# Optimization experiments

Hardware: AMD Instinct MI355X
Metric: run time of the kernel (lower is better)

## Reference

```python
import jax, jax.numpy as jnp
import numpy as np

MAX_FRAMES = 12
EMBED_DIM = 512
TOPK = 12
NUM_SAMPLES = 500
SIGMA = 0.05
SEL_DIM = 2
NUM_HEADS = 2


def setup_inputs() -> dict:
    key = jax.random.key(0)
    ks = jax.random.split(key, 9)
    D = EMBED_DIM
    C = D // 2
    s = lambda fan_in: 1.0 / np.sqrt(fan_in)
    return {
        "x": jax.random.normal(ks[0], (16, MAX_FRAMES * 50, D), dtype=jnp.float32),
        "ln_g": jnp.ones((D,), jnp.float32),
        "ln_b": jnp.zeros((D,), jnp.float32),
        "w_in": jax.random.normal(ks[1], (D, C), jnp.float32) * s(D),
        "wq": jax.random.normal(ks[2], (C, C), jnp.float32) * s(C),
        "wk": jax.random.normal(ks[3], (C, C), jnp.float32) * s(C),
        "wv": jax.random.normal(ks[4], (C, C), jnp.float32) * s(C),
        "wo": jax.random.normal(ks[5], (C, C), jnp.float32) * s(C),
        "w1": jax.random.normal(ks[6], (2 * C, C), jnp.float32) * s(2 * C),
        "w2": jax.random.normal(ks[7], (C, 1), jnp.float32) * s(C),
    }


def layer_norm(x, g, b, eps=1e-5):
    mu = jnp.mean(x, axis=-1, keepdims=True)
    var = jnp.var(x, axis=-1, keepdims=True)
    return (x - mu) * jax.lax.rsqrt(var + eps) * g + b


def mha(x, wq, wk, wv, wo):
    B, N, C = x.shape
    hd = C // NUM_HEADS
    q = (x @ wq).reshape(B, N, NUM_HEADS, hd).transpose(0, 2, 1, 3)
    k = (x @ wk).reshape(B, N, NUM_HEADS, hd).transpose(0, 2, 1, 3)
    v = (x @ wv).reshape(B, N, NUM_HEADS, hd).transpose(0, 2, 1, 3)
    attn = jax.nn.softmax(jnp.einsum('bhnd,bhmd->bhnm', q, k) / np.sqrt(hd), axis=-1)
    out = jnp.einsum('bhnm,bhmd->bhnd', attn, v).transpose(0, 2, 1, 3).reshape(B, N, C)
    return out @ wo


def predictor(x, ln_g, ln_b, w_in, wq, wk, wv, wo, w1, w2):
    h = jax.nn.gelu(layer_norm(x, ln_g, ln_b) @ w_in, approximate=False)
    h = mha(h, wq, wk, wv, wo)
    B, N, C = h.shape
    g = jnp.mean(h, axis=1, keepdims=True)
    h = jnp.concatenate([h, jnp.broadcast_to(g, (B, N, C))], axis=-1)
    h = jax.nn.gelu(h @ w1, approximate=False)
    return jnp.tanh(h @ w2)  # (B, N, 1)


def perturbed_topk(scores):
    # scores: (b, d) -> soft indicators (b, k, d)
    b, d = scores.shape
    noise = jax.random.normal(jax.random.key(1), (b, NUM_SAMPLES, d), dtype=scores.dtype)
    perturbed = scores[:, None, :] + noise * SIGMA
    _, idx = jax.lax.top_k(perturbed, TOPK)            # (b, ns, k)
    idx = jnp.sort(idx, axis=-1)
    onehot = jax.nn.one_hot(idx, d, dtype=scores.dtype)  # (b, ns, k, d)
    return onehot.mean(axis=1)                          # (b, k, d)


def reference(x, ln_g, ln_b, w_in, wq, wk, wv, wo, w1, w2):
    B, L, D = x.shape
    N = L // MAX_FRAMES
    xf = x.reshape(B * MAX_FRAMES, N, D)
    pred = predictor(xf, ln_g, ln_b, w_in, wq, wk, wv, wo, w1, w2)[..., 0]  # (b, N)
    spatial_score = pred[:, SEL_DIM:]                    # (b, N-2)
    ind = perturbed_topk(spatial_score)                  # (b, k, N-2)
    cls_feat = xf[:, :SEL_DIM, :]
    spatial_feat = xf[:, SEL_DIM:, :]
    sel = jnp.einsum('bkl,bld->bkd', ind, spatial_feat)
    out = jnp.concatenate([cls_feat, sel], axis=1)       # (b, 2+k, D)
    return out.reshape(B, -1, D)
```

## Files before the change

### kernel.cpp

```cpp
#include <hip/hip_runtime.h>
#include <stdint.h>

#define B2      192
#define NTOK    50
#define ROWS    9600
#define D_EMB   512
#define C_DIM   256
#define HD      128
#define NSAMP   500
#define TOPKK   12
#define NSPA    48

typedef short short8 __attribute__((ext_vector_type(8)));
typedef float f32x4  __attribute__((ext_vector_type(4)));

__device__ __forceinline__ float gelu_f(float x) {
    return 0.5f * x * (1.0f + erff(x * 0.7071067811865476f));
}
__device__ __forceinline__ uint16_t f2bf(float x) {
    uint32_t u = __float_as_uint(x);
    return (uint16_t)((u + 0x7fffu + ((u >> 16) & 1u)) >> 16);
}
__device__ __forceinline__ float bf2f(uint16_t b) {
    return __uint_as_float(((uint32_t)b) << 16);
}
__device__ __forceinline__ size_t swzA(int m, int k, int K) {
    return ((size_t)(m >> 4) * (K >> 5) + (k >> 5)) * 512
         + (size_t)((((k >> 3) & 3) * 16 + (m & 15)) * 8 + (k & 7));
}

__global__ __launch_bounds__(256) void prep_kernel(const float* __restrict__ x,
                                                   const float* __restrict__ g,
                                                   const float* __restrict__ b,
                                                   short* __restrict__ xh,
                                                   short* __restrict__ xl,
                                                   const float* __restrict__ w_in, const float* __restrict__ wq,
                                                   const float* __restrict__ wk, const float* __restrict__ wv,
                                                   const float* __restrict__ wo, const float* __restrict__ w1,
                                                   short* win_hi, short* win_lo, short* wq_hi, short* wq_lo,
                                                   short* wk_hi, short* wk_lo, short* wv_hi, short* wv_lo,
                                                   short* wo_hi, short* wo_lo, short* w1a_hi, short* w1a_lo,
                                                   short* w1b_hi, short* w1b_lo) {
    if (blockIdx.x < 2400) {
        int row  = blockIdx.x * 4 + (threadIdx.x >> 6);
        int lane = threadIdx.x & 63;
        const float* rp = x + (size_t)row * D_EMB;
        float4 v0 = *(const float4*)(rp + lane * 8);
        float4 v1 = *(const float4*)(rp + lane * 8 + 4);
        float s  = v0.x + v0.y + v0.z + v0.w + v1.x + v1.y + v1.z + v1.w;
        float s2 = v0.x*v0.x + v0.y*v0.y + v0.z*v0.z + v0.w*v0.w
                 + v1.x*v1.x + v1.y*v1.y + v1.z*v1.z + v1.w*v1.w;
#pragma unroll
        for (int off = 32; off; off >>= 1) {
            s  += __shfl_xor(s,  off);
            s2 += __shfl_xor(s2, off);
        }
        float mu  = s / 512.0f;
        float var = s2 / 512.0f - mu * mu;
        float inv = 1.0f / sqrtf(var + 1e-5f);
        const float* gp = g + lane * 8;
        const float* bp = b + lane * 8;
        float o[8];
        o[0]=(v0.x-mu)*inv*gp[0]+bp[0]; o[1]=(v0.y-mu)*inv*gp[1]+bp[1];
        o[2]=(v0.z-mu)*inv*gp[2]+bp[2]; o[3]=(v0.w-mu)*inv*gp[3]+bp[3];
        o[4]=(v1.x-mu)*inv*gp[4]+bp[4]; o[5]=(v1.y-mu)*inv*gp[5]+bp[5];
        o[6]=(v1.z-mu)*inv*gp[6]+bp[6]; o[7]=(v1.w-mu)*inv*gp[7]+bp[7];
        short8 h8, l8;
#pragma unroll
        for (int j = 0; j < 8; ++j) {
            uint16_t h = f2bf(o[j]);
            h8[j] = (short)h;
            l8[j] = (short)f2bf(o[j] - bf2f(h));
        }
        size_t blk = (size_t)(row >> 4) * 16 + (lane >> 2);
        int inner  = (lane & 3) * 16 + (row & 15);
        ((short8*)xh)[blk * 64 + inner] = h8;
        ((short8*)xl)[blk * 64 + inner] = l8;
    } else {
        int blk = blockIdx.x - 2400;
        const float* W; short *hi, *lo; int K, base;
        if      (blk <  64) { W = w_in;            hi = win_hi; lo = win_lo; K = 512; base = 0;   }
        else if (blk <  96) { W = wq;              hi = wq_hi;  lo = wq_lo;  K = 256; base = 64;  }
        else if (blk < 128) { W = wk;              hi = wk_hi;  lo = wk_lo;  K = 256; base = 96;  }
        else if (blk < 160) { W = wv;              hi = wv_hi;  lo = wv_lo;  K = 256; base = 128; }
        else if (blk < 192) { W = wo;              hi = wo_hi;  lo = wo_lo;  K = 256; base = 160; }
        else if (blk < 224) { W = w1;              hi = w1a_hi; lo = w1a_lo; K = 256; base = 192; }
        else                { W = w1 + 256 * 256;  hi = w1b_hi; lo = w1b_lo; K = 256; base = 224; }
        int t = (blk - base) * 256 + threadIdx.x;
        int n = t & 255, k8 = t >> 8;
        short8 h8, l8;
#pragma unroll
        for (int j = 0; j < 8; ++j) {
            float wvl = W[(size_t)(k8 * 8 + j) * 256 + n];
            uint16_t h = f2bf(wvl);
            h8[j] = (short)h;
            l8[j] = (short)f2bf(wvl - bf2f(h));
        }
        size_t bb = (size_t)(n >> 4) * (K >> 5) + (k8 >> 2);
        int inner = (k8 & 3) * 16 + (n & 15);
        ((short8*)hi)[bb * 64 + inner] = h8;
        ((short8*)lo)[bb * 64 + inner] = l8;
    }
}

template<int KB>
__device__ __forceinline__ void mm_core(const short8* __restrict__ pAh, const short8* __restrict__ pAl,
                                        const short8* __restrict__ pBh0, const short8* __restrict__ pBl0,
                                        const short8* __restrict__ pBh1, const short8* __restrict__ pBl1,
                                        f32x4& acc0, f32x4& acc1) {
    short8 ah[3], al[3], bh0[3], bl0[3], bh1[3], bl1[3];
#pragma unroll
    for (int i = 0; i < 2; ++i) {
        int off = i * 64;
        ah[i] = pAh[off];  al[i] = pAl[off];
        bh0[i] = pBh0[off]; bl0[i] = pBl0[off];
        bh1[i] = pBh1[off]; bl1[i] = pBl1[off];
    }
#pragma unroll
    for (int ks = 0; ks < KB; ++ks) {
        int cur = ks % 3;
        if (ks + 2 < KB) {
            int pre = (ks + 2) % 3, off = (ks + 2) * 64;
            ah[pre] = pAh[off];  al[pre] = pAl[off];
            bh0[pre] = pBh0[off]; bl0[pre] = pBl0[off];
            bh1[pre] = pBh1[off]; bl1[pre] = pBl1[off];
        }
        acc0 = __builtin_amdgcn_mfma_f32_16x16x32_bf16(ah[cur], bh0[cur], acc0, 0, 0, 0);
        acc0 = __builtin_amdgcn_mfma_f32_16x16x32_bf16(ah[cur], bl0[cur], acc0, 0, 0, 0);
        acc0 = __builtin_amdgcn_mfma_f32_16x16x32_bf16(al[cur], bh0[cur], acc0, 0, 0, 0);
        acc1 = __builtin_amdgcn_mfma_f32_16x16x32_bf16(ah[cur], bh1[cur], acc1, 0, 0, 0);
        acc1 = __builtin_amdgcn_mfma_f32_16x16x32_bf16(ah[cur], bl1[cur], acc1, 0, 0, 0);
        acc1 = __builtin_amdgcn_mfma_f32_16x16x32_bf16(al[cur], bh1[cur], acc1, 0, 0, 0);
    }
}

__device__ __forceinline__ void epi_store(f32x4 acc, int row0, int col, int N,
                                          float* __restrict__ Cf, short* __restrict__ Chi,
                                          short* __restrict__ Clo,
                                          const float* __restrict__ bias, int act) {
#pragma unroll
    for (int r = 0; r < 4; ++r) {
        int row = row0 + r;
        float v2 = acc[r];
        if (bias) v2 += bias[(size_t)(row / 50) * N + col];
        if (act)  v2 = gelu_f(v2);
        if (Cf) Cf[(size_t)row * N + col] = v2;
        if (Chi) {
            uint16_t h = f2bf(v2);
            size_t ad = swzA(row, col, 256);
            Chi[ad] = (short)h;
            Clo[ad] = (short)f2bf(v2 - bf2f(h));
        }
    }
}

template<int KB>
__global__ __launch_bounds__(256) void gemm_one(const short8* __restrict__ Ah,
                                                const short8* __restrict__ Al,
                                                const short8* __restrict__ Bh,
                                                const short8* __restrict__ Bl,
                                                float* __restrict__ Cf,
                                                short* __restrict__ Chi,
                                                short* __restrict__ Clo,
                                                const float* __restrict__ bias,
                                                int act) {
    int lane = threadIdx.x & 63;
    int wv   = threadIdx.x >> 6;
    int ms   = blockIdx.x * 4 + wv;
    int ns0  = blockIdx.y * 2;
    const short8* pAh  = Ah + (size_t)ms  * KB * 64 + lane;
    const short8* pAl  = Al + (size_t)ms  * KB * 64 + lane;
    const short8* pBh0 = Bh + (size_t)ns0 * KB * 64 + lane;
    const short8* pBl0 = Bl + (size_t)ns0 * KB * 64 + lane;
    const short8* pBh1 = pBh0 + (size_t)KB * 64;
    const short8* pBl1 = pBl0 + (size_t)KB * 64;
    f32x4 acc0 = {0.f,0.f,0.f,0.f}, acc1 = {0.f,0.f,0.f,0.f};
    mm_core<KB>(pAh, pAl, pBh0, pBl0, pBh1, pBl1, acc0, acc1);
    int row0 = ms * 16 + (lane >> 4) * 4;
    int cin  = lane & 15;
    epi_store(acc0, row0, ns0 * 16 + cin,      256, Cf, Chi, Clo, bias, act);
    epi_store(acc1, row0, (ns0 + 1) * 16 + cin, 256, Cf, Chi, Clo, bias, act);
}

__global__ __launch_bounds__(256) void gemm_qkv(const short8* __restrict__ Ah,
                                                const short8* __restrict__ Al,
                                                const short8* __restrict__ Bhq, const short8* __restrict__ Blq,
                                                const short8* __restrict__ Bhk, const short8* __restrict__ Blk,
                                                const short8* __restrict__ Bhv, const short8* __restrict__ Blv,
                                                float* __restrict__ q, float* __restrict__ k,
                                                float* __restrict__ v) {
    int lane = threadIdx.x & 63;
    int wv   = threadIdx.x >> 6;
    int ms   = blockIdx.x * 4 + wv;
    int sel  = blockIdx.y >> 3;
    int ns0  = (blockIdx.y & 7) * 2;
    const short8* Bh = (sel == 0) ? Bhq : (sel == 1) ? Bhk : Bhv;
    const short8* Bl = (sel == 0) ? Blq : (sel == 1) ? Blk : Blv;
    float* C = (sel == 0) ? q : (sel == 1) ? k : v;
    const short8* pAh  = Ah + (size_t)ms  * 8 * 64 + lane;
    const short8* pAl  = Al + (size_t)ms  * 8 * 64 + lane;
    const short8* pBh0 = Bh + (size_t)ns0 * 8 * 64 + lane;
    const short8* pBl0 = Bl + (size_t)ns0 * 8 * 64 + lane;
    const short8* pBh1 = pBh0 + 8 * 64;
    const short8* pBl1 = pBl0 + 8 * 64;
    f32x4 acc0 = {0.f,0.f,0.f,0.f}, acc1 = {0.f,0.f,0.f,0.f};
    mm_core<8>(pAh, pAl, pBh0, pBl0, pBh1, pBl1, acc0, acc1);
    int row0 = ms * 16 + (lane >> 4) * 4;
    int cin  = lane & 15;
    epi_store(acc0, row0, ns0 * 16 + cin,      256, C, nullptr, nullptr, nullptr, 0);
    epi_store(acc1, row0, (ns0 + 1) * 16 + cin, 256, C, nullptr, nullptr, nullptr, 0);
}

__global__ __launch_bounds__(256) void attn_kernel(const float* __restrict__ q,
                                                   const float* __restrict__ k,
                                                   const float* __restrict__ v,
                                                   short* __restrict__ aoh,
                                                   short* __restrict__ aol) {
    __shared__ float sQ[NTOK * 132];
    __shared__ float sK[NTOK * 132];
    __shared__ float sS[NTOK * 51];
    int blk = blockIdx.x;
    int b = blk >> 1, h = blk & 1;
    const size_t base = (size_t)b * NTOK * C_DIM + h * HD;
    int tid = threadIdx.x;
    for (int idx = tid; idx < 1600; idx += 256) {
        int r = idx >> 5, c = (idx & 31) * 4;
        *(float4*)&sQ[r * 132 + c] = *(const float4*)(q + base + (size_t)r * C_DIM + c);
        *(float4*)&sK[r * 132 + c] = *(const float4*)(k + base + (size_t)r * C_DIM + c);
    }
    __syncthreads();
    for (int e = tid; e < 625; e += 256) {
        int i2 = e / 25, j2 = e - i2 * 25;
        int i = i2 * 2, j = j2 * 2;
        const float* qi0 = &sQ[i * 132];
        const float* qi1 = qi0 + 132;
        const float* kj0 = &sK[j * 132];
        const float* kj1 = kj0 + 132;
        float4 a00 = {0,0,0,0}, a01 = {0,0,0,0}, a10 = {0,0,0,0}, a11 = {0,0,0,0};
#pragma unroll
        for (int t = 0; t < 32; ++t) {
            float4 q0 = *(const float4*)&qi0[t * 4];
            float4 q1 = *(const float4*)&qi1[t * 4];
            float4 b0 = *(const float4*)&kj0[t * 4];
            float4 b1 = *(const float4*)&kj1[t * 4];
            a00.x = fmaf(q0.x, b0.x, a00.x); a00.y = fmaf(q0.y, b0.y, a00.y);
            a00.z = fmaf(q0.z, b0.z, a00.z); a00.w = fmaf(q0.w, b0.w, a00.w);
            a01.x = fmaf(q0.x, b1.x, a01.x); a01.y = fmaf(q0.y, b1.y, a01.y);
            a01.z = fmaf(q0.z, b1.z, a01.z); a01.w = fmaf(q0.w, b1.w, a01.w);
            a10.x = fmaf(q1.x, b0.x, a10.x); a10.y = fmaf(q1.y, b0.y, a10.y);
            a10.z = fmaf(q1.z, b0.z, a10.z); a10.w = fmaf(q1.w, b0.w, a10.w);
            a11.x = fmaf(q1.x, b1.x, a11.x); a11.y = fmaf(q1.y, b1.y, a11.y);
            a11.z = fmaf(q1.z, b1.z, a11.z); a11.w = fmaf(q1.w, b1.w, a11.w);
        }
        const float sc = 0.08838834764831845f;
        sS[i * 51 + j]           = (a00.x + a00.y + a00.z + a00.w) * sc;
        sS[i * 51 + j + 1]       = (a01.x + a01.y + a01.z + a01.w) * sc;
        sS[(i + 1) * 51 + j]     = (a10.x + a10.y + a10.z + a10.w) * sc;
        sS[(i + 1) * 51 + j + 1] = (a11.x + a11.y + a11.z + a11.w) * sc;
    }
    __syncthreads();
    for (int idx = tid; idx < 1600; idx += 256) {
        int r = idx >> 5, c = (idx & 31) * 4;
        *(float4*)&sQ[r * 132 + c] = *(const float4*)(v + base + (size_t)r * C_DIM + c);
    }
    if (tid < NTOK) {
        float* row = &sS[tid * 51];
        float m = row[0];
        for (int j = 1; j < NTOK; ++j) m = fmaxf(m, row[j]);
        float sum = 0.f;
        for (int j = 0; j < NTOK; ++j) { float e2 = expf(row[j] - m); row[j] = e2; sum += e2; }
        float inv = 1.0f / sum;
        for (int j = 0; j < NTOK; ++j) row[j] *= inv;
    }
    __syncthreads();
    for (int e = tid; e < 1600; e += 256) {
        int i = e >> 5, d4 = (e & 31) * 4;
        const float* srow = &sS[i * 51];
        float4 acc = {0,0,0,0};
#pragma unroll
        for (int j = 0; j < NTOK; ++j) {
            float w = srow[j];
            float4 v4 = *(const float4*)&sQ[j * 132 + d4];
            acc.x = fmaf(w, v4.x, acc.x); acc.y = fmaf(w, v4.y, acc.y);
            acc.z = fmaf(w, v4.z, acc.z); acc.w = fmaf(w, v4.w, acc.w);
        }
        int row = b * NTOK + i;
        float vals[4] = {acc.x, acc.y, acc.z, acc.w};
#pragma unroll
        for (int c = 0; c < 4; ++c) {
            int col = h * HD + d4 + c;
            uint16_t hh = f2bf(vals[c]);
            size_t ad = swzA(row, col, 256);
            aoh[ad] = (short)hh;
            aol[ad] = (short)f2bf(vals[c] - bf2f(hh));
        }
    }
}

__global__ __launch_bounds__(256) void mean50(const float* __restrict__ h2,
                                              short* __restrict__ gh,
                                              short* __restrict__ gl) {
    int b = blockIdx.x, c = threadIdx.x;
    float s = 0.f;
    for (int n = 0; n < NTOK; ++n) s += h2[((size_t)b * NTOK + n) * C_DIM + c];
    float g = s / 50.0f;
    uint16_t h = f2bf(g);
    size_t ad = swzA(b, c, 256);
    gh[ad] = (short)h;
    gl[ad] = (short)f2bf(g - bf2f(h));
}

__global__ __launch_bounds__(256) void matvec_tanh(const float* __restrict__ h3,
                                                   const float* __restrict__ w2,
                                                   float* __restrict__ pred) {
    int row  = blockIdx.x * 4 + (threadIdx.x >> 6);
    int lane = threadIdx.x & 63;
    const float* rp = h3 + (size_t)row * C_DIM;
    float4 a = *(const float4*)(rp + lane * 4);
    float4 w = *(const float4*)(w2 + lane * 4);
    float s = a.x * w.x + a.y * w.y + a.z * w.z + a.w * w.w;
#pragma unroll
    for (int off = 32; off; off >>= 1) s += __shfl_xor(s, off);
    if (lane == 0) pred[row] = tanhf(s);
}

__device__ __forceinline__ uint32_t rotl32(uint32_t x, int r) {
    return (x << r) | (x >> (32 - r));
}
__device__ __forceinline__ void threefry01(uint32_t& x0, uint32_t& x1) {
    const uint32_t ks0 = 0u, ks1 = 1u, ks2 = 0x1BD11BDBu;
    x0 += ks0; x1 += ks1;
#define TFR(r) { x0 += x1; x1 = rotl32(x1, r); x1 ^= x0; }
    TFR(13) TFR(15) TFR(26) TFR(6)  x0 += ks1; x1 += ks2 + 1u;
    TFR(17) TFR(29) TFR(16) TFR(24) x0 += ks2; x1 += ks0 + 2u;
    TFR(13) TFR(15) TFR(26) TFR(6)  x0 += ks0; x1 += ks1 + 3u;
    TFR(17) TFR(29) TFR(16) TFR(24) x0 += ks1; x1 += ks2 + 4u;
    TFR(13) TFR(15) TFR(26) TFR(6)  x0 += ks2; x1 += ks0 + 5u;
#undef TFR
}

__device__ __forceinline__ float erfinv_xla(float x) {
    float w = -log1pf(-x * x);
    float p;
    if (w < 5.0f) {
        w -= 2.5f;
        p = 2.81022636e-08f;
        p = fmaf(p, w, 3.43273939e-07f);
        p = fmaf(p, w, -3.5233877e-06f);
        p = fmaf(p, w, -4.39150654e-06f);
        p = fmaf(p, w, 0.00021858087f);
        p = fmaf(p, w, -0.00125372503f);
        p = fmaf(p, w, -0.00417768164f);
        p = fmaf(p, w, 0.246640727f);
        p = fmaf(p, w, 1.50140941f);
    } else {
        w = sqrtf(w) - 3.0f;
        p = -0.000200214257f;
        p = fmaf(p, w, 0.000100950558f);
        p = fmaf(p, w, 0.00134934322f);
        p = fmaf(p, w, -0.00367342844f);
        p = fmaf(p, w, 0.00573950773f);
        p = fmaf(p, w, -0.0076224613f);
        p = fmaf(p, w, 0.00943887047f);
        p = fmaf(p, w, 1.00167406f);
        p = fmaf(p, w, 2.83297682f);
    }
    return p * x;
}

__device__ __forceinline__ float bits_to_normal(uint32_t bits) {
    float f = __uint_as_float((bits >> 9) | 0x3f800000u) - 1.0f;
    float u = f * 2.0f + (-0.99999994039535522461f);
    u = fmaxf(-0.99999994039535522461f, u);
    return 1.4142135623730951f * erfinv_xla(u);
}

__global__ __launch_bounds__(256) void topk_kernel(const float* __restrict__ pred,
                                                   int* __restrict__ counts) {
    __shared__ unsigned long long sK[128][13];
    int lane = threadIdx.x & 63;
    int wv   = threadIdx.x >> 6;
    int p    = wv >> 1;
    int hh   = wv & 1;
    int g    = blockIdx.x * 128 + p * 64 + lane;
    int b    = g / NSAMP;
    int s    = g - b * NSAMP;
    uint32_t base = (uint32_t)((b * NSAMP + s) * NSPA);
    const float* sp = pred + b * NTOK + 2;

    unsigned long long list[TOPKK];
#pragma unroll
    for (int i = 0; i < TOPKK; ++i) list[i] = 0ull;

    int d0 = hh * 24;
#pragma unroll 2
    for (int dd = 0; dd < 24; ++dd) {
        int d = d0 + dd;
        uint32_t x0 = 0u, x1 = base + (uint32_t)d;
        threefry01(x0, x1);
        float n  = bits_to_normal(x0 ^ x1);
        float v  = sp[d] + n * 0.05f;
        uint32_t vb   = __float_as_uint(v);
        uint32_t mono = (vb & 0x80000000u) ? ~vb : (vb | 0x80000000u);
        unsigned long long key = ((unsigned long long)mono << 6) | (unsigned)(63 - d);
#pragma unroll
        for (int i = 0; i < TOPKK; ++i) {
            bool gt = key > list[i];
            unsigned long long mx = gt ? key : list[i];
            unsigned long long mn = gt ? list[i] : key;
            list[i] = mx; key = mn;
        }
    }
    int rowL = p * 64 + lane;
    if (hh == 1) {
#pragma unroll
        for (int i = 0; i < TOPKK; ++i) sK[rowL][i] = list[i];
    }
    __syncthreads();
    if (hh == 0) {
        unsigned long long M[TOPKK];
#pragma unroll
        for (int i = 0; i < TOPKK; ++i) {
            unsigned long long o = sK[rowL][11 - i];
            M[i] = (list[i] > o) ? list[i] : o;
        }
        unsigned long long m = 0ull;
#pragma unroll
        for (int i = 0; i < TOPKK; ++i) m |= 1ull << (unsigned)(M[i] & 63ull);
#pragma unroll
        for (int i = 0; i < TOPKK; ++i) {
            unsigned a = (unsigned)(M[i] & 63ull);
            int kpos = 11 - __popcll(m & ((1ull << a) - 1ull));
            int d    = 63 - (int)a;
            atomicAdd(&counts[((size_t)b * TOPKK + kpos) * NSPA + d], 1);
        }
    }
}

__global__ __launch_bounds__(256) void select_out(const float* __restrict__ x,
                                                  const int* __restrict__ counts,
                                                  float* __restrict__ out) {
    int row = blockIdx.x;
    int b = row / 14, k = row - b * 14;
    int d = threadIdx.x;
    if (k < 2) {
        out[(size_t)row * D_EMB + d]       = x[((size_t)(b * NTOK + k)) * D_EMB + d];
        out[(size_t)row * D_EMB + d + 256] = x[((size_t)(b * NTOK + k)) * D_EMB + d + 256];
    } else {
        int kk = k - 2;
        const int* cnt = counts + ((size_t)b * TOPKK + kk) * NSPA;
        __shared__ int sc[NSPA];
        if (d < NSPA) sc[d] = cnt[d];
        __syncthreads();
        float a0 = 0.f, a1 = 0.f;
        for (int l = 0; l < NSPA; ++l) {
            int c = sc[l];
            if (c) {
                float w = (float)c / 500.0f;
                const float* xr = x + ((size_t)(b * NTOK + 2 + l)) * D_EMB;
                a0 = fmaf(w, xr[d], a0);
                a1 = fmaf(w, xr[d + 256], a1);
            }
        }
        out[(size_t)row * D_EMB + d]       = a0;
        out[(size_t)row * D_EMB + d + 256] = a1;
    }
}

extern "C" void kernel_launch(void* const* d_in, const int* in_sizes, int n_in,
                              void* d_out, int out_size, void* d_ws, size_t ws_size,
                              hipStream_t stream) {
    const float* x    = (const float*)d_in[0];
    const float* ln_g = (const float*)d_in[1];
    const float* ln_b = (const float*)d_in[2];
    const float* w_in = (const float*)d_in[3];
    const float* wq   = (const float*)d_in[4];
    const float* wk   = (const float*)d_in[5];
    const float* wv   = (const float*)d_in[6];
    const float* wo   = (const float*)d_in[7];
    const float* w1   = (const float*)d_in[8];
    const float* w2   = (const float*)d_in[9];
    float* out = (float*)d_out;

    char* W = (char*)d_ws;
    short* xn_hi  = (short*)(W + 0);
    short* xn_lo  = (short*)(W + 9830400);
    short* ao_hi  = (short*)(W + 0);
    short* ao_lo  = (short*)(W + 4915200);
    short* h2_hi  = (short*)(W + 9830400);
    short* h2_lo  = (short*)(W + 14745600);
    short* h1_hi  = (short*)(W + 19660800);
    short* h1_lo  = (short*)(W + 24576000);
    float* h3     = (float*)(W + 19660800);
    float* q      = (float*)(W + 29491200);
    float* h2f    = (float*)(W + 29491200);
    float* k      = (float*)(W + 39321600);
    float* v      = (float*)(W + 49152000);
    short* win_hi = (short*)(W + 58982400);
    short* win_lo = (short*)(W + 59244544);
    short* wq_hi  = (short*)(W + 59506688);
    short* wq_lo  = (short*)(W + 59637760);
    short* wk_hi  = (short*)(W + 59768832);
    short* wk_lo  = (short*)(W + 59899904);
    short* wv_hi  = (short*)(W + 60030976);
    short* wv_lo  = (short*)(W + 60162048);
    short* wo_hi  = (short*)(W + 60293120);
    short* wo_lo  = (short*)(W + 60424192);
    short* w1a_hi = (short*)(W + 60555264);
    short* w1a_lo = (short*)(W + 60686336);
    short* w1b_hi = (short*)(W + 60817408);
    short* w1b_lo = (short*)(W + 60948480);
    short* gm_hi  = (short*)(W + 61079552);
    short* gm_lo  = (short*)(W + 61177856);
    float* gw     = (float*)(W + 61276160);
    float* pred   = (float*)(W + 61472768);
    int*   counts = (int*)  (W + 61511168);

    hipMemsetAsync(counts, 0, (size_t)B2 * TOPKK * NSPA * sizeof(int), stream);
    prep_kernel<<<2656, 256, 0, stream>>>(x, ln_g, ln_b, xn_hi, xn_lo,
        w_in, wq, wk, wv, wo, w1,
        win_hi, win_lo, wq_hi, wq_lo, wk_hi, wk_lo, wv_hi, wv_lo,
        wo_hi, wo_lo, w1a_hi, w1a_lo, w1b_hi, w1b_lo);
    gemm_one<16><<<dim3(150, 8), 256, 0, stream>>>((const short8*)xn_hi, (const short8*)xn_lo,
        (const short8*)win_hi, (const short8*)win_lo, nullptr, h1_hi, h1_lo, nullptr, 1);
    gemm_qkv<<<dim3(150, 24), 256, 0, stream>>>((const short8*)h1_hi, (const short8*)h1_lo,
        (const short8*)wq_hi, (const short8*)wq_lo, (const short8*)wk_hi, (const short8*)wk_lo,
        (const short8*)wv_hi, (const short8*)wv_lo, q, k, v);
    attn_kernel<<<B2 * 2, 256, 0, stream>>>(q, k, v, ao_hi, ao_lo);
    gemm_one<8><<<dim3(150, 8), 256, 0, stream>>>((const short8*)ao_hi, (const short8*)ao_lo,
        (const short8*)wo_hi, (const short8*)wo_lo, h2f, h2_hi, h2_lo, nullptr, 0);
    mean50<<<B2, 256, 0, stream>>>(h2f, gm_hi, gm_lo);
    gemm_one<8><<<dim3(3, 8), 256, 0, stream>>>((const short8*)gm_hi, (const short8*)gm_lo,
        (const short8*)w1b_hi, (const short8*)w1b_lo, gw, nullptr, nullptr, nullptr, 0);
    gemm_one<8><<<dim3(150, 8), 256, 0, stream>>>((const short8*)h2_hi, (const short8*)h2_lo,
        (const short8*)w1a_hi, (const short8*)w1a_lo, h3, nullptr, nullptr, gw, 1);
    matvec_tanh<<<ROWS / 4, 256, 0, stream>>>(h3, w2, pred);
    topk_kernel<<<750, 256, 0, stream>>>(pred, counts);
    select_out<<<B2 * 14, 256, 0, stream>>>(x, counts, out);
}
```

Before: 297.4 us.

## Use 32-bit top-k keys with threshold-based selection and split atomic emission

The per-thread top-12 insertion list now uses 32-bit monotone keys instead of 64-bit keys with packed indices, which halves compare and select cost in the insertion chain. Each half-wave's candidate keys are kept in shared memory. The merged 12th-largest threshold is computed from both halves, and each half then counts and emits its selected indices in order, handling ties by index order. Both halves now issue atomics instead of one, at the cost of extra shared-memory traffic and a second barrier.

```diff
diff --git a/kernel.cpp b/kernel.cpp
--- a/kernel.cpp
+++ b/kernel.cpp
@@ -375,11 +375,20 @@
     return 1.4142135623730951f * erfinv_xla(u);
 }
 
-__global__ __launch_bounds__(256) void topk_kernel(const float* __restrict__ pred,
-                                                   int* __restrict__ counts) {
-    __shared__ unsigned long long sK[128][13];
-    int lane = threadIdx.x & 63;
-    int wv   = threadIdx.x >> 6;
+#define INS_U32(li) { bool gt = key > (li); uint32_t mx = gt ? key : (li); \
+                      key = gt ? (li) : key; (li) = mx; }
+#define INS12_U32() { INS_U32(q0) INS_U32(q1) INS_U32(q2) INS_U32(q3) \
+                      INS_U32(q4) INS_U32(q5) INS_U32(q6) INS_U32(q7) \
+                      INS_U32(q8) INS_U32(q9) INS_U32(q10) INS_U32(q11) }
+
+__global__ __launch_bounds__(256) __attribute__((amdgpu_waves_per_eu(2, 8)))
+void topk_kernel(const float* __restrict__ pred, int* __restrict__ counts) {
+    __shared__ uint32_t sM[256][25];
+    __shared__ uint32_t sL[256][13];
+    __shared__ uint32_t sC[256][2];
+    int tid  = threadIdx.x;
+    int lane = tid & 63;
+    int wv   = tid >> 6;
     int p    = wv >> 1;
     int hh   = wv & 1;
     int g    = blockIdx.x * 128 + p * 64 + lane;
@@ -387,53 +396,67 @@
     int s    = g - b * NSAMP;
     uint32_t base = (uint32_t)((b * NSAMP + s) * NSPA);
     const float* sp = pred + b * NTOK + 2;
-
-    unsigned long long list[TOPKK];
-#pragma unroll
-    for (int i = 0; i < TOPKK; ++i) list[i] = 0ull;
-
     int d0 = hh * 24;
+
+    uint32_t q0=0,q1=0,q2=0,q3=0,q4=0,q5=0,q6=0,q7=0,q8=0,q9=0,q10=0,q11=0;
+
 #pragma unroll 2
     for (int dd = 0; dd < 24; ++dd) {
-        int d = d0 + dd;
-        uint32_t x0 = 0u, x1 = base + (uint32_t)d;
+        uint32_t x0 = 0u, x1 = base + (uint32_t)(d0 + dd);
         threefry01(x0, x1);
         float n  = bits_to_normal(x0 ^ x1);
-        float v  = sp[d] + n * 0.05f;
-        uint32_t vb   = __float_as_uint(v);
-        uint32_t mono = (vb & 0x80000000u) ? ~vb : (vb | 0x80000000u);
-        unsigned long long key = ((unsigned long long)mono << 6) | (unsigned)(63 - d);
-#pragma unroll
-        for (int i = 0; i < TOPKK; ++i) {
-            bool gt = key > list[i];
-            unsigned long long mx = gt ? key : list[i];
-            unsigned long long mn = gt ? list[i] : key;
-            list[i] = mx; key = mn;
-        }
-    }
-    int rowL = p * 64 + lane;
-    if (hh == 1) {
-#pragma unroll
-        for (int i = 0; i < TOPKK; ++i) sK[rowL][i] = list[i];
-    }
+        float v  = sp[d0 + dd] + n * 0.05f;
+        uint32_t vb  = __float_as_uint(v);
+        uint32_t key = (vb & 0x80000000u) ? ~vb : (vb | 0x80000000u);
+        sM[tid][dd] = key;
+        INS12_U32()
+    }
+    sL[tid][0] = q0;  sL[tid][1] = q1;  sL[tid][2]  = q2;  sL[tid][3]  = q3;
+    sL[tid][4] = q4;  sL[tid][5] = q5;  sL[tid][6]  = q6;  sL[tid][7]  = q7;
+    sL[tid][8] = q8;  sL[tid][9] = q9;  sL[tid][10] = q10; sL[tid][11] = q11;
     __syncthreads();
-    if (hh == 0) {
-        unsigned long long M[TOPKK];
-#pragma unroll
-        for (int i = 0; i < TOPKK; ++i) {
-            unsigned long long o = sK[rowL][11 - i];
-            M[i] = (list[i] > o) ? list[i] : o;
-        }
-        unsigned long long m = 0ull;
-#pragma unroll
-        for (int i = 0; i < TOPKK; ++i) m |= 1ull << (unsigned)(M[i] & 63ull);
-#pragma unroll
-        for (int i = 0; i < TOPKK; ++i) {
-            unsigned a = (unsigned)(M[i] & 63ull);
-            int kpos = 11 - __popcll(m & ((1ull << a) - 1ull));
-            int d    = 63 - (int)a;
-            atomicAdd(&counts[((size_t)b * TOPKK + kpos) * NSPA + d], 1);
-        }
+
+    const uint32_t* PL = sL[tid ^ 64];
+    uint32_t t, mx;
+    mx = q0  > PL[11] ? q0  : PL[11]; t = mx;
+    mx = q1  > PL[10] ? q1  : PL[10]; t = mx < t ? mx : t;
+    mx = q2  > PL[9]  ? q2  : PL[9];  t = mx < t ? mx : t;
+    mx = q3  > PL[8]  ? q3  : PL[8];  t = mx < t ? mx : t;
+    mx = q4  > PL[7]  ? q4  : PL[7];  t = mx < t ? mx : t;
+    mx = q5  > PL[6]  ? q5  : PL[6];  t = mx < t ? mx : t;
+    mx = q6  > PL[5]  ? q6  : PL[5];  t = mx < t ? mx : t;
+    mx = q7  > PL[4]  ? q7  : PL[4];  t = mx < t ? mx : t;
+    mx = q8  > PL[3]  ? q8  : PL[3];  t = mx < t ? mx : t;
+    mx = q9  > PL[2]  ? q9  : PL[2];  t = mx < t ? mx : t;
+    mx = q10 > PL[1]  ? q10 : PL[1];  t = mx < t ? mx : t;
+    mx = q11 > PL[0]  ? q11 : PL[0];  t = mx < t ? mx : t;
+
+    int cgt = 0, ceq = 0;
+#pragma unroll 4
+    for (int dd = 0; dd < 24; ++dd) {
+        uint32_t m = sM[tid][dd];
+        cgt += (m > t) ? 1 : 0;
+        ceq += (m == t) ? 1 : 0;
+    }
+    sC[tid][0] = (uint32_t)cgt;
+    sC[tid][1] = (uint32_t)ceq;
+    __syncthreads();
+
+    int cgt_o = (int)sC[tid ^ 64][0];
+    int ceq_o = (int)sC[tid ^ 64][1];
+    int r = TOPKK - (cgt + cgt_o);
+    int eqBase  = hh ? ceq_o : 0;
+    int selBase = hh ? (cgt_o + (ceq_o < r ? ceq_o : r)) : 0;
+    int run = 0, eqRun = 0;
+    size_t cb = (size_t)b * TOPKK;
+#pragma unroll 4
+    for (int dd = 0; dd < 24; ++dd) {
+        uint32_t m = sM[tid][dd];
+        bool isEq = (m == t);
+        bool sel  = (m > t) || (isEq && (eqBase + eqRun) < r);
+        if (sel) atomicAdd(&counts[(cb + selBase + run) * NSPA + (d0 + dd)], 1);
+        run   += sel  ? 1 : 0;
+        eqRun += isEq ? 1 : 0;
     }
 }
 
```

New measurement: 326.7 us. +9.9%, slower.
